# Performance work log

Measured on AMD Instinct MI355X. Metric: run time of the kernel, lower is better.

The kernel has to match this reference:

```python
import jax, jax.numpy as jnp
import numpy as np

K_SECTIONS = 8


def _make_sos(K=K_SECTIONS, seed=0):
    """Build K stable biquad sections [K, 6] = [b0,b1,b2,a0,a1,a2], unit DC gain."""
    rng = np.random.default_rng(seed)
    r_p = rng.uniform(0.5, 0.95, K)
    th_p = rng.uniform(0.1, 3.0, K)
    r_z = rng.uniform(0.5, 0.99, K)
    th_z = rng.uniform(0.1, 3.0, K)
    a1 = -2.0 * r_p * np.cos(th_p)
    a2 = r_p ** 2
    b1 = -2.0 * r_z * np.cos(th_z)
    b2 = r_z ** 2
    b0 = np.ones(K)
    g = (1.0 + a1 + a2) / (b0 + b1 + b2)  # normalize DC gain to 1 per section
    sos = np.stack([b0 * g, b1 * g, b2 * g, np.ones(K), a1, a2], axis=1)
    return jnp.asarray(sos, dtype=jnp.float32)


def setup_inputs() -> dict:
    key = jax.random.key(0)
    x = jax.random.normal(key, (128, 65536), dtype=jnp.float32)  # [C, T]
    return {"x": x, "sos": _make_sos()}


def reference(x, sos):
    """Fused SOS cascade: sequential direct-form-I biquad recurrence over time."""
    K = sos.shape[0]
    a0 = sos[:, 3]
    b0, b1, b2 = sos[:, 0] / a0, sos[:, 1] / a0, sos[:, 2] / a0  # [K]
    a1, a2 = sos[:, 4] / a0, sos[:, 5] / a0                      # [K]
    C, T = x.shape

    def step(carry, xt):  # xt: [C]
        x1, x2, y1, y2 = carry  # each [K, C]
        s = xt
        nx1, nx2, ny1, ny2 = [], [], [], []
        for k in range(K):  # fixed small unroll over cascaded sections
            y = (b0[k] * s + b1[k] * x1[k] + b2[k] * x2[k]
                 - a1[k] * y1[k] - a2[k] * y2[k])
            nx2.append(x1[k]); nx1.append(s)
            ny2.append(y1[k]); ny1.append(y)
            s = y
        carry = (jnp.stack(nx1), jnp.stack(nx2), jnp.stack(ny1), jnp.stack(ny2))
        return carry, s

    init = tuple(jnp.zeros((K, C), x.dtype) for _ in range(4))
    _, y = jax.lax.scan(step, init, x.T)  # scan over time axis -> y: [T, C]
    return y.T
```

## Files before the change

kernel.cpp:

```cpp
#include <hip/hip_runtime.h>


#define T_LEN   65536
#define CG      16
#define TB      1024
#define NTAP    144
#define HALO    128
#define XSPAN   (HALO + TB + 32)
#define XSTRIDE 1192
#define NQ4     (CG * (XSPAN / 4))
#define Q4ROW   (XSPAN / 4)
#define TPB     512
#define NSTAGE  (TPB - 64)

typedef _Float16 half8  __attribute__((ext_vector_type(8)));
typedef _Float16 half4h __attribute__((ext_vector_type(4)));
typedef float    f32x4  __attribute__((ext_vector_type(4)));

__global__ __launch_bounds__(TPB)
void FusedSOSCascade_20040317403806_kernel(const float* __restrict__ x,
                                           const float* __restrict__ sos,
                                           float* __restrict__ out) {
  __shared__ alignas(16) _Float16 lds_x[CG * XSTRIDE];
  __shared__ alignas(16) float hs[NTAP];
  __shared__ alignas(16) _Float16 atab[64 * 5 * 8];

  const int tid = threadIdx.x;
  const int cg  = blockIdx.x & 7;
  const int tb  = blockIdx.x >> 3;
  const int c0  = cg * CG;
  const int t0  = tb * TB;

  if (tid < 64) {
    const int k = tid & 7;
    {
      const float a0  = sos[k * 6 + 3];
      const float cb0 =  sos[k * 6 + 0] / a0;
      const float cb1 =  sos[k * 6 + 1] / a0;
      const float cb2 =  sos[k * 6 + 2] / a0;
      const float cn1 = -(sos[k * 6 + 4] / a0);
      const float cn2 = -(sos[k * 6 + 5] / a0);
      float y = 0.f, z1 = 0.f, z2 = 0.f;
#pragma unroll 4
      for (int n = 0; n < NTAP + 7; ++n) {
        const int ui = __builtin_amdgcn_update_dpp(0, __float_as_int(y),
                                                   0x111, 0xf, 0xf, true);
        float s = __int_as_float(ui);
        if (tid == 0) s = (n == 0) ? 1.f : 0.f;
        y  = fmaf(cb0, s, z1);
        z1 = fmaf(cb1, s, fmaf(cn1, y, z2));
        z2 = fmaf(cb2, s, cn2 * y);
        if (tid == 7 && n >= 7) hs[n - 7] = y;
      }
    }
    asm volatile("s_waitcnt lgkmcnt(0)" ::: "memory");
    {
      const int r = tid & 15, g = tid >> 4;
#pragma unroll
      for (int m = 0; m < 5; ++m) {
        half8 af;
#pragma unroll
        for (int e = 0; e < 8; ++e) {
          const int i = r + 128 - 32 * m - 8 * g - e;
          const float hv = (i >= 0 && i < NTAP) ? hs[i] : 0.f;
          af[e] = (_Float16)hv;
        }
        *(half8*)(&atab[(tid * 5 + m) * 8]) = af;
      }
    }
  } else {
    const int st = tid - 64;
#pragma unroll 1
    for (int k0 = 0; k0 < 11; k0 += 6) {
      float4 v[6];
      const int kn = (k0 == 0) ? 6 : 5;
#pragma unroll
      for (int j = 0; j < 6; ++j) {
        if (j < kn) {
          const int idx = st + (k0 + j) * NSTAGE;
          float4 t = make_float4(0.f, 0.f, 0.f, 0.f);
          if (idx < NQ4) {
            const int row = idx / Q4ROW;
            const int c4  = idx - row * Q4ROW;
            const int gt  = t0 - HALO + 4 * c4;
            if (gt >= 0 && gt < T_LEN)
              t = *(const float4*)(x + (size_t)(c0 + row) * T_LEN + gt);
          }
          v[j] = t;
        }
      }
#pragma unroll
      for (int j = 0; j < 6; ++j) {
        if (j < kn) {
          const int idx = st + (k0 + j) * NSTAGE;
          if (idx < NQ4) {
            const int row = idx / Q4ROW;
            const int c4  = idx - row * Q4ROW;
            half4h hv = { (_Float16)v[j].x, (_Float16)v[j].y,
                          (_Float16)v[j].z, (_Float16)v[j].w };
            *(half4h*)(&lds_x[row * XSTRIDE + 4 * c4]) = hv;
          }
        }
      }
    }
  }
  __syncthreads();

  const int wv = tid >> 6;
  const int l  = tid & 63;
  const int r  = l & 15;
  const int g  = l >> 4;

  half8 afrag[5];
#pragma unroll
  for (int m = 0; m < 5; ++m)
    afrag[m] = *(const half8*)(&atab[(l * 5 + m) * 8]);

#define XFRAG(tt, m) \
  (*(const half8*)(&lds_x[r * XSTRIDE + 16 * (tt) + 32 * (m) + 8 * g]))

  const int te = wv * 8;
  float* orow = out + (size_t)(c0 + r) * T_LEN + t0;

  half8 E[5], O[5];
#pragma unroll
  for (int m = 0; m < 5; ++m) E[m] = XFRAG(te, m);
#pragma unroll
  for (int m = 0; m < 5; ++m) O[m] = XFRAG(te + 1, m);

#pragma unroll
  for (int q = 0; q < 4; ++q) {
    f32x4 accE = {0.f, 0.f, 0.f, 0.f};
    f32x4 accO = {0.f, 0.f, 0.f, 0.f};
#pragma unroll
    for (int m = 0; m < 5; ++m) {
      accE = __builtin_amdgcn_mfma_f32_16x16x32_f16(afrag[m], E[m], accE,
                                                    0, 0, 0);
      accO = __builtin_amdgcn_mfma_f32_16x16x32_f16(afrag[m], O[m], accO,
                                                    0, 0, 0);
    }
    const int ttE = te + 2 * q;
    *(float4*)(orow + 16 * ttE + 4 * g) =
        make_float4(accE[0], accE[1], accE[2], accE[3]);
    *(float4*)(orow + 16 * (ttE + 1) + 4 * g) =
        make_float4(accO[0], accO[1], accO[2], accO[3]);
    if (q < 3) {
#pragma unroll
      for (int m = 0; m < 4; ++m) { E[m] = E[m + 1]; O[m] = O[m + 1]; }
      E[4] = XFRAG(ttE + 2, 4);
      O[4] = XFRAG(ttE + 3, 4);
    }
  }
#undef XFRAG
}

extern "C" void kernel_launch(void* const* d_in, const int* in_sizes, int n_in,
                              void* d_out, int out_size, void* d_ws, size_t ws_size,
                              hipStream_t stream) {
  const float* x   = (const float*)d_in[0];
  const float* sos = (const float*)d_in[1];
  float* out = (float*)d_out;
  (void)in_sizes; (void)n_in; (void)out_size; (void)d_ws; (void)ws_size;

  FusedSOSCascade_20040317403806_kernel<<<dim3(512), dim3(TPB), 0, stream>>>(
      x, sos, out);
}
```

Before: 87.44 us.

## Split tap build into separate kernel and load inputs directly from global

Moves the impulse-response/A-fragment table construction into a tiny separate kernel that writes to workspace. The main kernel no longer stages input into LDS behind a block barrier. Each wave now loads its own fp32 input windows from global, converts them to fp16 in registers, and prefetches the next fragments while the MFMAs run. Blocks shrink to 256 threads and the grid doubles to 1024. This removes the serial per-block IIR setup and the barrier stall, but adds a second launch and re-reads overlapping halo data from global/cache instead of sharing it through LDS.

```diff
diff --git a/kernel.cpp b/kernel.cpp
--- a/kernel.cpp
+++ b/kernel.cpp
@@ -1,135 +1,101 @@
 #include <hip/hip_runtime.h>
 
 
-#define T_LEN   65536
-#define CG      16
-#define TB      1024
-#define NTAP    144
-#define HALO    128
-#define XSPAN   (HALO + TB + 32)
-#define XSTRIDE 1192
-#define NQ4     (CG * (XSPAN / 4))
-#define Q4ROW   (XSPAN / 4)
-#define TPB     512
-#define NSTAGE  (TPB - 64)
+#define T_LEN 65536
+#define NTAP  144
+#define TPB   256
 
-typedef _Float16 half8  __attribute__((ext_vector_type(8)));
-typedef _Float16 half4h __attribute__((ext_vector_type(4)));
-typedef float    f32x4  __attribute__((ext_vector_type(4)));
+typedef _Float16 half8 __attribute__((ext_vector_type(8)));
+typedef float    f32x4 __attribute__((ext_vector_type(4)));
 
-__global__ __launch_bounds__(TPB)
+__global__ __launch_bounds__(64)
+void FusedSOS_hbuild(const float* __restrict__ sos,
+                     _Float16* __restrict__ atab) {
+  __shared__ float hs[NTAP];
+  const int tid = threadIdx.x;
+  const int k = tid & 7;
+  const float a0  = sos[k * 6 + 3];
+  const float cb0 =  sos[k * 6 + 0] / a0;
+  const float cb1 =  sos[k * 6 + 1] / a0;
+  const float cb2 =  sos[k * 6 + 2] / a0;
+  const float cn1 = -(sos[k * 6 + 4] / a0);
+  const float cn2 = -(sos[k * 6 + 5] / a0);
+  float y = 0.f, z1 = 0.f, z2 = 0.f;
+#pragma unroll 4
+  for (int n = 0; n < NTAP + 7; ++n) {
+    const int ui = __builtin_amdgcn_update_dpp(0, __float_as_int(y),
+                                               0x111, 0xf, 0xf, true);
+    float s = __int_as_float(ui);
+    if (tid == 0) s = (n == 0) ? 1.f : 0.f;
+    y  = fmaf(cb0, s, z1);
+    z1 = fmaf(cb1, s, fmaf(cn1, y, z2));
+    z2 = fmaf(cb2, s, cn2 * y);
+    if (tid == 7 && n >= 7) hs[n - 7] = y;
+  }
+  asm volatile("s_waitcnt lgkmcnt(0)" ::: "memory");
+  const int r = tid & 15, g = tid >> 4;
+#pragma unroll
+  for (int m = 0; m < 5; ++m) {
+    half8 af;
+#pragma unroll
+    for (int e = 0; e < 8; ++e) {
+      const int i = r + 128 - 32 * m - 8 * g - e;
+      af[e] = (_Float16)((i >= 0 && i < NTAP) ? hs[i] : 0.f);
+    }
+    *(half8*)(&atab[(tid * 5 + m) * 8]) = af;
+  }
+}
+
+#define LOADF(dst, OFF)                                                      \
+  do {                                                                       \
+    const int off_ = (OFF);                                                  \
+    float4 aa = make_float4(0.f, 0.f, 0.f, 0.f);                             \
+    float4 bb = make_float4(0.f, 0.f, 0.f, 0.f);                             \
+    if (off_ >= 0 && off_ < T_LEN) {                                         \
+      aa = *(const float4*)(xr + off_);                                      \
+      bb = *(const float4*)(xr + off_ + 4);                                  \
+    }                                                                        \
+    (dst) = (half8){(_Float16)aa.x, (_Float16)aa.y, (_Float16)aa.z,          \
+                    (_Float16)aa.w, (_Float16)bb.x, (_Float16)bb.y,          \
+                    (_Float16)bb.z, (_Float16)bb.w};                         \
+  } while (0)
+
+__global__ __launch_bounds__(TPB, 4)
 void FusedSOSCascade_20040317403806_kernel(const float* __restrict__ x,
-                                           const float* __restrict__ sos,
+                                           const _Float16* __restrict__ atab,
                                            float* __restrict__ out) {
-  __shared__ alignas(16) _Float16 lds_x[CG * XSTRIDE];
-  __shared__ alignas(16) float hs[NTAP];
-  __shared__ alignas(16) _Float16 atab[64 * 5 * 8];
+  const int tid = threadIdx.x;
+  const int wv  = tid >> 6;
+  const int l   = tid & 63;
+  const int r   = l & 15;
+  const int g   = l >> 4;
+  const int cgi = blockIdx.x >> 7;
+  const int tb  = blockIdx.x & 127;
+  const int c0  = cgi * 16;
+  const int tstart = tb * 512 + wv * 128;
 
-  const int tid = threadIdx.x;
-  const int cg  = blockIdx.x & 7;
-  const int tb  = blockIdx.x >> 3;
-  const int c0  = cg * CG;
-  const int t0  = tb * TB;
-
-  if (tid < 64) {
-    const int k = tid & 7;
-    {
-      const float a0  = sos[k * 6 + 3];
-      const float cb0 =  sos[k * 6 + 0] / a0;
-      const float cb1 =  sos[k * 6 + 1] / a0;
-      const float cb2 =  sos[k * 6 + 2] / a0;
-      const float cn1 = -(sos[k * 6 + 4] / a0);
-      const float cn2 = -(sos[k * 6 + 5] / a0);
-      float y = 0.f, z1 = 0.f, z2 = 0.f;
-#pragma unroll 4
-      for (int n = 0; n < NTAP + 7; ++n) {
-        const int ui = __builtin_amdgcn_update_dpp(0, __float_as_int(y),
-                                                   0x111, 0xf, 0xf, true);
-        float s = __int_as_float(ui);
-        if (tid == 0) s = (n == 0) ? 1.f : 0.f;
-        y  = fmaf(cb0, s, z1);
-        z1 = fmaf(cb1, s, fmaf(cn1, y, z2));
-        z2 = fmaf(cb2, s, cn2 * y);
-        if (tid == 7 && n >= 7) hs[n - 7] = y;
-      }
-    }
-    asm volatile("s_waitcnt lgkmcnt(0)" ::: "memory");
-    {
-      const int r = tid & 15, g = tid >> 4;
-#pragma unroll
-      for (int m = 0; m < 5; ++m) {
-        half8 af;
-#pragma unroll
-        for (int e = 0; e < 8; ++e) {
-          const int i = r + 128 - 32 * m - 8 * g - e;
-          const float hv = (i >= 0 && i < NTAP) ? hs[i] : 0.f;
-          af[e] = (_Float16)hv;
-        }
-        *(half8*)(&atab[(tid * 5 + m) * 8]) = af;
-      }
-    }
-  } else {
-    const int st = tid - 64;
-#pragma unroll 1
-    for (int k0 = 0; k0 < 11; k0 += 6) {
-      float4 v[6];
-      const int kn = (k0 == 0) ? 6 : 5;
-#pragma unroll
-      for (int j = 0; j < 6; ++j) {
-        if (j < kn) {
-          const int idx = st + (k0 + j) * NSTAGE;
-          float4 t = make_float4(0.f, 0.f, 0.f, 0.f);
-          if (idx < NQ4) {
-            const int row = idx / Q4ROW;
-            const int c4  = idx - row * Q4ROW;
-            const int gt  = t0 - HALO + 4 * c4;
-            if (gt >= 0 && gt < T_LEN)
-              t = *(const float4*)(x + (size_t)(c0 + row) * T_LEN + gt);
-          }
-          v[j] = t;
-        }
-      }
-#pragma unroll
-      for (int j = 0; j < 6; ++j) {
-        if (j < kn) {
-          const int idx = st + (k0 + j) * NSTAGE;
-          if (idx < NQ4) {
-            const int row = idx / Q4ROW;
-            const int c4  = idx - row * Q4ROW;
-            half4h hv = { (_Float16)v[j].x, (_Float16)v[j].y,
-                          (_Float16)v[j].z, (_Float16)v[j].w };
-            *(half4h*)(&lds_x[row * XSTRIDE + 4 * c4]) = hv;
-          }
-        }
-      }
-    }
-  }
-  __syncthreads();
-
-  const int wv = tid >> 6;
-  const int l  = tid & 63;
-  const int r  = l & 15;
-  const int g  = l >> 4;
+  const float* xr = x + (size_t)(c0 + r) * T_LEN;
 
   half8 afrag[5];
 #pragma unroll
   for (int m = 0; m < 5; ++m)
     afrag[m] = *(const half8*)(&atab[(l * 5 + m) * 8]);
 
-#define XFRAG(tt, m) \
-  (*(const half8*)(&lds_x[r * XSTRIDE + 16 * (tt) + 32 * (m) + 8 * g]))
-
-  const int te = wv * 8;
-  float* orow = out + (size_t)(c0 + r) * T_LEN + t0;
-
+  const int base = tstart + 8 * g - 128;
   half8 E[5], O[5];
 #pragma unroll
-  for (int m = 0; m < 5; ++m) E[m] = XFRAG(te, m);
+  for (int m = 0; m < 5; ++m) LOADF(E[m], base + 32 * m);
 #pragma unroll
-  for (int m = 0; m < 5; ++m) O[m] = XFRAG(te + 1, m);
+  for (int m = 0; m < 5; ++m) LOADF(O[m], base + 16 + 32 * m);
 
+  float* orow = out + (size_t)(c0 + r) * T_LEN + tstart;
 #pragma unroll
   for (int q = 0; q < 4; ++q) {
+    half8 nE, nO;
+    if (q < 3) {
+      LOADF(nE, base + 160 + 32 * q);
+      LOADF(nO, base + 176 + 32 * q);
+    }
     f32x4 accE = {0.f, 0.f, 0.f, 0.f};
     f32x4 accO = {0.f, 0.f, 0.f, 0.f};
 #pragma unroll
@@ -139,19 +105,16 @@
       accO = __builtin_amdgcn_mfma_f32_16x16x32_f16(afrag[m], O[m], accO,
                                                     0, 0, 0);
     }
-    const int ttE = te + 2 * q;
-    *(float4*)(orow + 16 * ttE + 4 * g) =
+    *(float4*)(orow + 32 * q + 4 * g) =
         make_float4(accE[0], accE[1], accE[2], accE[3]);
-    *(float4*)(orow + 16 * (ttE + 1) + 4 * g) =
+    *(float4*)(orow + 32 * q + 16 + 4 * g) =
         make_float4(accO[0], accO[1], accO[2], accO[3]);
     if (q < 3) {
 #pragma unroll
       for (int m = 0; m < 4; ++m) { E[m] = E[m + 1]; O[m] = O[m + 1]; }
-      E[4] = XFRAG(ttE + 2, 4);
-      O[4] = XFRAG(ttE + 3, 4);
+      E[4] = nE; O[4] = nO;
     }
   }
-#undef XFRAG
 }
 
 extern "C" void kernel_launch(void* const* d_in, const int* in_sizes, int n_in,
@@ -160,8 +123,10 @@
   const float* x   = (const float*)d_in[0];
   const float* sos = (const float*)d_in[1];
   float* out = (float*)d_out;
-  (void)in_sizes; (void)n_in; (void)out_size; (void)d_ws; (void)ws_size;
+  _Float16* atab = (_Float16*)d_ws;
+  (void)in_sizes; (void)n_in; (void)out_size; (void)ws_size;
 
-  FusedSOSCascade_20040317403806_kernel<<<dim3(512), dim3(TPB), 0, stream>>>(
-      x, sos, out);
+  FusedSOS_hbuild<<<dim3(1), dim3(64), 0, stream>>>(sos, atab);
+  FusedSOSCascade_20040317403806_kernel<<<dim3(1024), dim3(TPB), 0, stream>>>(
+      x, atab, out);
 }
```

After: 100.5 us. 14.9% more time.
